# Kernel optimization log

Hardware: AMD Instinct MI355X
Metric: run time of the kernel (lower is better)

## Reference

```python
import jax, jax.numpy as jnp
import numpy as np

B, L, C, H = 4, 2048, 512, 8
D = C // H  # head_dim = 64


def _rope_tables(L, D):
    inv_freq = 1.0 / (10000.0 ** (np.arange(0, D, 2, dtype=np.float32) / D))
    t = np.arange(L, dtype=np.float32)
    freqs = np.outer(t, inv_freq)                      # (L, D/2)
    emb = np.concatenate([freqs, freqs], axis=-1)      # (L, D)
    return jnp.asarray(np.cos(emb)), jnp.asarray(np.sin(emb))


def setup_inputs() -> dict:
    key = jax.random.key(0)
    k1, k2, k3 = jax.random.split(key, 3)
    cos, sin = _rope_tables(L, D)
    return {
        "x": jax.random.normal(k1, (B, L, C), dtype=jnp.float32),
        "qkv_w": jax.random.normal(k2, (3 * C, C), dtype=jnp.float32) * 0.02,
        "qkv_b": jnp.zeros((3 * C,), dtype=jnp.float32),
        "proj_w": jax.random.normal(k3, (C, C), dtype=jnp.float32) * 0.02,
        "proj_b": jnp.zeros((C,), dtype=jnp.float32),
        "cos": cos,
        "sin": sin,
    }


def _rotate_half(x):
    x1, x2 = jnp.split(x, 2, axis=-1)
    return jnp.concatenate([-x2, x1], axis=-1)


def _apply_rope(x, cos, sin):
    # x: (B, H, L, D); cos/sin: (L, D)
    return x * cos[None, None] + _rotate_half(x) * sin[None, None]


def reference(x, qkv_w, qkv_b, proj_w, proj_b, cos, sin):
    b, l, c = x.shape
    scale = 1.0 / jnp.sqrt(jnp.float32(D))
    qkv = x @ qkv_w.T + qkv_b                          # (B, L, 3C)
    qkv = qkv.reshape(b, l, 3, H, D).transpose(2, 0, 3, 1, 4)  # (3, B, H, L, D)
    q, k, v = qkv[0], qkv[1], qkv[2]
    q = _apply_rope(q, cos, sin)
    k = _apply_rope(k, cos, sin)
    attn = jax.nn.softmax(scale * jnp.einsum('bhqd,bhkd->bhqk', q, k), axis=-1)
    out = jnp.einsum('bhqk,bhkd->bhqd', attn, v)       # (B, H, L, D)
    out = out.transpose(0, 2, 1, 3).reshape(b, l, c)   # (B, L, C)
    return out @ proj_w.T + proj_b
```

## Files before the change

### kernel.cpp

```cpp
#include <hip/hip_runtime.h>

#define CDIM 512
#define LDIM 2048
#define BDIM 4
#define HDIM 8
#define DDIM 64

typedef __attribute__((ext_vector_type(8))) short bf16x8;
typedef __attribute__((ext_vector_type(4))) float f32x4;
typedef __attribute__((ext_vector_type(2))) float f32x2;
typedef __attribute__((ext_vector_type(8))) unsigned short ushort8;

static __device__ __forceinline__ unsigned short f2bf(float f) {
  unsigned u = __float_as_uint(f);
  return (unsigned short)((u + 0x7FFFu + ((u >> 16) & 1u)) >> 16);
}

__global__ __launch_bounds__(256) void convert_kernel(
    const float* __restrict__ qw, const float* __restrict__ pw,
    unsigned short* __restrict__ wb, unsigned short* __restrict__ pwb) {
  const size_t i = ((size_t)blockIdx.x * 256 + threadIdx.x) * 8;
  const float* src; unsigned short* dst; size_t off;
  if (i < 786432) { src = qw; dst = wb;  off = i; }
  else            { src = pw; dst = pwb; off = i - 786432; }
  const float4 a = *(const float4*)(src + off);
  const float4 b = *(const float4*)(src + off + 4);
  ushort8 h;
  h[0] = f2bf(a.x); h[1] = f2bf(a.y); h[2] = f2bf(a.z); h[3] = f2bf(a.w);
  h[4] = f2bf(b.x); h[5] = f2bf(b.y); h[6] = f2bf(b.z); h[7] = f2bf(b.w);
  *(ushort8*)(dst + off) = h;
}

__global__ __launch_bounds__(256) void qkv_gemm_kernel(
    const float* __restrict__ x, const unsigned short* __restrict__ wb,
    const float* __restrict__ bias, const float* __restrict__ cosT,
    const float* __restrict__ sinT, unsigned short* __restrict__ qb,
    unsigned short* __restrict__ kb, unsigned short* __restrict__ vt) {
  __shared__ char As[16384];
  __shared__ char Bs[16384];
  const int t  = threadIdx.x;
  const int w  = t >> 6, lane = t & 63;
  const int lo = lane & 15, hi = lane >> 4;
  const int wm = w >> 1, wn = w & 1;
  const int m0 = blockIdx.y * 128, n0 = blockIdx.x * 128;

  f32x4 acc[4][4];
  #pragma unroll
  for (int mt = 0; mt < 4; ++mt)
    #pragma unroll
    for (int nt = 0; nt < 4; ++nt) acc[mt][nt] = (f32x4){0.f, 0.f, 0.f, 0.f};

  const int srow   = t >> 3;
  const int sch    = (t & 7) ^ (srow & 7);
  const char* Bg = (const char*)wb;

  for (int kt = 0; kt < CDIM; kt += 64) {
    #pragma unroll
    for (int s = 0; s < 4; ++s) {
      const int r = s * 32 + srow;
      const float4 f0 = *(const float4*)(x + (size_t)(m0 + r) * CDIM + kt + sch * 8);
      const float4 f1 = *(const float4*)(x + (size_t)(m0 + r) * CDIM + kt + sch * 8 + 4);
      unsigned u0, u1, u2, u3;
      asm("v_cvt_pk_bf16_f32 %0, %1, %2" : "=v"(u0) : "v"(f0.x), "v"(f0.y));
      asm("v_cvt_pk_bf16_f32 %0, %1, %2" : "=v"(u1) : "v"(f0.z), "v"(f0.w));
      asm("v_cvt_pk_bf16_f32 %0, %1, %2" : "=v"(u2) : "v"(f1.x), "v"(f1.y));
      asm("v_cvt_pk_bf16_f32 %0, %1, %2" : "=v"(u3) : "v"(f1.z), "v"(f1.w));
      uint4 uu; uu.x = u0; uu.y = u1; uu.z = u2; uu.w = u3;
      *(uint4*)(As + s * 4096 + t * 16) = uu;
      __builtin_amdgcn_global_load_lds(
          (const __attribute__((address_space(1))) unsigned int*)
              (Bg + (size_t)(n0 + r) * 1024 + kt * 2 + sch * 16),
          (__attribute__((address_space(3))) unsigned int*)(Bs + s * 4096 + w * 1024),
          16, 0, 0);
    }
    __syncthreads();
    #pragma unroll
    for (int ks = 0; ks < 2; ++ks) {
      bf16x8 af[4], bfr[4];
      #pragma unroll
      for (int mt = 0; mt < 4; ++mt)
        af[mt] = *(const bf16x8*)(As + (wm * 64 + mt * 16 + lo) * 128
                                  + (((ks * 4 + hi) ^ (lo & 7)) << 4));
      #pragma unroll
      for (int nt = 0; nt < 4; ++nt)
        bfr[nt] = *(const bf16x8*)(Bs + (wn * 64 + nt * 16 + lo) * 128
                                   + (((ks * 4 + hi) ^ (lo & 7)) << 4));
      #pragma unroll
      for (int mt = 0; mt < 4; ++mt)
        #pragma unroll
        for (int nt = 0; nt < 4; ++nt)
          acc[mt][nt] = __builtin_amdgcn_mfma_f32_16x16x32_bf16(
              af[mt], bfr[nt], acc[mt][nt], 0, 0, 0);
    }
    __syncthreads();
  }

  const int nbase = n0 + wn * 64;
  const int typ   = nbase >> 9;
  const int hh    = (nbase >> 6) & 7;
  const int bb    = m0 >> 11;
  const int lbase = (m0 & 2047) + wm * 64;

  float bq[4];
  #pragma unroll
  for (int nt = 0; nt < 4; ++nt) bq[nt] = bias[nbase + nt * 16 + lo];
  #pragma unroll
  for (int mt = 0; mt < 4; ++mt)
    #pragma unroll
    for (int nt = 0; nt < 4; ++nt)
      #pragma unroll
      for (int reg = 0; reg < 4; ++reg) acc[mt][nt][reg] += bq[nt];

  if (typ == 2) {
    unsigned short* vbase = vt + (size_t)(bb * HDIM + hh) * DDIM * LDIM;
    #pragma unroll
    for (int mt = 0; mt < 4; ++mt)
      #pragma unroll
      for (int nt = 0; nt < 4; ++nt) {
        const int d = nt * 16 + lo;
        #pragma unroll
        for (int reg = 0; reg < 4; ++reg) {
          const int l = lbase + mt * 16 + hi * 4 + reg;
          vbase[(size_t)d * LDIM + l] = f2bf(acc[mt][nt][reg]);
        }
      }
  } else {
    unsigned short* dstb = (typ ? kb : qb) + (size_t)(bb * HDIM + hh) * LDIM * DDIM;
    #pragma unroll
    for (int mt = 0; mt < 4; ++mt)
      #pragma unroll
      for (int nt = 0; nt < 4; ++nt) {
        const int d   = nt * 16 + lo;
        const float sgn = (nt & 2) ? 1.f : -1.f;
        #pragma unroll
        for (int reg = 0; reg < 4; ++reg) {
          const int l = lbase + mt * 16 + hi * 4 + reg;
          const float c = cosT[l * 64 + d], s = sinT[l * 64 + d];
          const float v = acc[mt][nt][reg] * c + sgn * acc[mt][nt ^ 2][reg] * s;
          dstb[(size_t)l * DDIM + d] = f2bf(v);
        }
      }
  }
}

#define CLOG2 0.18033688f

__global__ __launch_bounds__(512, 4) void attn_kernel(
    unsigned short* __restrict__ qb, const unsigned short* __restrict__ kb,
    const unsigned short* __restrict__ vt) {
  __shared__ char Lds[65536];
  const int t    = threadIdx.x;
  const int w    = t >> 6, lane = t & 63;
  const int lo   = lane & 15, hi = lane >> 4;
  const int wq   = w & 3, half = w >> 2;
  const int bh   = blockIdx.y;
  const int q0   = blockIdx.x * 128 + wq * 32;
  const int kb0  = half * 1024;

  const char* Kb = (const char*)kb + (size_t)bh * (LDIM * DDIM * 2);
  const char* Vb = (const char*)vt + (size_t)bh * (LDIM * DDIM * 2);
  unsigned short* Qb = qb + (size_t)bh * (LDIM * DDIM);

  bf16x8 qf[2][2];
  #pragma unroll
  for (int g = 0; g < 2; ++g)
    #pragma unroll
    for (int kd = 0; kd < 2; ++kd)
      qf[g][kd] = *(const bf16x8*)((const char*)(Qb + (size_t)(q0 + g * 16 + lo) * DDIM)
                                   + kd * 64 + hi * 16);

  f32x4 o[2][4];
  float mrun[2] = {0.f, 0.f}, mc[2] = {0.f, 0.f}, lpart[2] = {0.f, 0.f};
  #pragma unroll
  for (int g = 0; g < 2; ++g)
    #pragma unroll
    for (int r = 0; r < 4; ++r) o[g][r] = (f32x4){0.f, 0.f, 0.f, 0.f};

  const int krow = wq * 8 + (lane >> 3);
  const int kch  = ((lane & 7) ^ (krow & 7)) << 4;
  const int vrow = wq * 16 + (lane >> 2);
  const int vch  = ((lane & 3) ^ (vrow & 3)) << 4;

  auto stage = [&](int tile, int buf) {
    __builtin_amdgcn_global_load_lds(
        (const __attribute__((address_space(1))) unsigned int*)
            (Kb + (size_t)(kb0 + tile * 32 + krow) * 128 + kch),
        (__attribute__((address_space(3))) unsigned int*)
            (Lds + (half * 2 + buf) * 4096 + wq * 1024),
        16, 0, 0);
    __builtin_amdgcn_global_load_lds(
        (const __attribute__((address_space(1))) unsigned int*)
            (Vb + (size_t)vrow * (LDIM * 2) + (size_t)(kb0 + tile * 32) * 2 + vch),
        (__attribute__((address_space(3))) unsigned int*)
            (Lds + 16384 + (half * 2 + buf) * 4096 + wq * 1024),
        16, 0, 0);
  };

  stage(0, 0);

  char* Pwb = Lds + 32768 + w * 4096;

  for (int kt = 0; kt < 32; ++kt) {
    const int cur = kt & 1;
    const int nk  = kt < 31 ? kt + 1 : 31;
    stage(nk, cur ^ 1);
    asm volatile("s_waitcnt vmcnt(2)");
    __builtin_amdgcn_s_barrier();
    __builtin_amdgcn_sched_barrier(0);

    const char* Kl = Lds + (half * 2 + cur) * 4096;
    const char* Vl = Lds + 16384 + (half * 2 + cur) * 4096;

    f32x4 sv[2][2];
    __builtin_amdgcn_s_setprio(1);
    #pragma unroll
    for (int nt = 0; nt < 2; ++nt) {
      sv[0][nt] = (f32x4){0.f, 0.f, 0.f, 0.f};
      sv[1][nt] = (f32x4){0.f, 0.f, 0.f, 0.f};
      const int key = nt * 16 + lo;
      #pragma unroll
      for (int kd = 0; kd < 2; ++kd) {
        const bf16x8 kf = *(const bf16x8*)(Kl + key * 128
                            + (((kd * 4 + hi) ^ (lo & 7)) << 4));
        sv[0][nt] = __builtin_amdgcn_mfma_f32_16x16x32_bf16(kf, qf[0][kd], sv[0][nt], 0, 0, 0);
        sv[1][nt] = __builtin_amdgcn_mfma_f32_16x16x32_bf16(kf, qf[1][kd], sv[1][nt], 0, 0, 0);
      }
    }
    __builtin_amdgcn_s_setprio(0);

    #pragma unroll
    for (int g = 0; g < 2; ++g) {
      const float* sflat = (const float*)sv[g];
      const f32x2 cc2 = {CLOG2, CLOG2};
      const f32x2 mm2 = {-mc[g], -mc[g]};
      float pv[8];
      float ps = 0.f;
      #pragma unroll
      for (int i = 0; i < 4; ++i) {
        f32x2 a; a[0] = sflat[2*i]; a[1] = sflat[2*i+1];
        f32x2 xr;
        asm("v_pk_fma_f32 %0, %1, %2, %3" : "=v"(xr) : "v"(a), "v"(cc2), "v"(mm2));
        float p0, p1;
        asm("v_exp_f32 %0, %1" : "=v"(p0) : "v"(xr[0]));
        asm("v_exp_f32 %0, %1" : "=v"(p1) : "v"(xr[1]));
        pv[2*i] = p0; pv[2*i+1] = p1;
        ps += p0; ps += p1;
      }

      if (__builtin_expect((bool)__ballot(ps > 65536.f), 0)) {
        float mx = -1e30f;
        #pragma unroll
        for (int i = 0; i < 8; ++i) mx = fmaxf(mx, sflat[i]);
        mx = fmaxf(mx, __shfl_xor(mx, 16));
        mx = fmaxf(mx, __shfl_xor(mx, 32));
        const float newm = fmaxf(mrun[g], mx);
        const float al   = exp2f((mrun[g] - newm) * CLOG2);
        lpart[g] *= al;
        #pragma unroll
        for (int r = 0; r < 4; ++r) {
          const float aq = __shfl(al, (hi << 2) + r);
          #pragma unroll
          for (int dt = 0; dt < 4; ++dt) o[g][dt][r] *= aq;
        }
        mrun[g] = newm;
        mc[g]   = newm * CLOG2;
        ps = 0.f;
        #pragma unroll
        for (int i = 0; i < 8; ++i) {
          const float p = exp2f(fmaf(sflat[i], CLOG2, -mc[g]));
          pv[i] = p;
          ps += p;
        }
      }
      lpart[g] += ps;

      #pragma unroll
      for (int nt = 0; nt < 2; ++nt) {
        unsigned w0, w1;
        asm("v_cvt_pk_bf16_f32 %0, %1, %2"
            : "=v"(w0) : "v"(pv[nt*4+0]), "v"(pv[nt*4+1]));
        asm("v_cvt_pk_bf16_f32 %0, %1, %2"
            : "=v"(w1) : "v"(pv[nt*4+2]), "v"(pv[nt*4+3]));
        uint2 d2; d2.x = w0; d2.y = w1;
        *(uint2*)(Pwb + g * 2048 + lo * 128
                  + ((nt * 32 + hi * 8) ^ ((lo & 7) << 4))) = d2;
      }
    }

    __builtin_amdgcn_s_setprio(1);
    {
      const bf16x8 pf0 = *(const bf16x8*)(Pwb + lo * 128
                           + ((hi ^ (lo & 7)) << 4));
      const bf16x8 pf1 = *(const bf16x8*)(Pwb + 2048 + lo * 128
                           + ((hi ^ (lo & 7)) << 4));
      #pragma unroll
      for (int dt = 0; dt < 4; ++dt) {
        const int d = dt * 16 + lo;
        const bf16x8 vf = *(const bf16x8*)(Vl + d * 64 + ((hi ^ (lo & 3)) << 4));
        o[0][dt] = __builtin_amdgcn_mfma_f32_16x16x32_bf16(pf0, vf, o[0][dt], 0, 0, 0);
        o[1][dt] = __builtin_amdgcn_mfma_f32_16x16x32_bf16(pf1, vf, o[1][dt], 0, 0, 0);
      }
    }
    __builtin_amdgcn_s_setprio(0);

    __builtin_amdgcn_sched_barrier(0);
    __builtin_amdgcn_s_barrier();
  }

  asm volatile("s_waitcnt vmcnt(0)");
  __syncthreads();

  float rs[2];
  #pragma unroll
  for (int g = 0; g < 2; ++g) {
    rs[g] = lpart[g];
    rs[g] += __shfl_xor(rs[g], 16);
    rs[g] += __shfl_xor(rs[g], 32);
  }

  if (half == 1) {
    #pragma unroll
    for (int g = 0; g < 2; ++g) {
      #pragma unroll
      for (int dt = 0; dt < 4; ++dt)
        #pragma unroll
        for (int r = 0; r < 4; ++r)
          *(float*)(Lds + wq * 8192
                    + ((g * 16 + hi * 4 + r) * 64 + dt * 16 + lo) * 4) = o[g][dt][r];
      if (hi == 0) {
        *(float*)(Lds + 32768 + wq * 256 + g * 64 + lo * 4)       = rs[g];
        *(float*)(Lds + 32768 + wq * 256 + 128 + g * 64 + lo * 4) = mrun[g];
      }
    }
  }
  __syncthreads();
  if (half == 0) {
    #pragma unroll
    for (int g = 0; g < 2; ++g)
      #pragma unroll
      for (int r = 0; r < 4; ++r) {
        const int qrow = hi * 4 + r;
        const float m_a = __shfl(mrun[g], qrow);
        const float l_a = __shfl(rs[g], qrow);
        const float l_b = *(const float*)(Lds + 32768 + wq * 256 + g * 64 + qrow * 4);
        const float m_b = *(const float*)(Lds + 32768 + wq * 256 + 128 + g * 64 + qrow * 4);
        const float m  = fmaxf(m_a, m_b);
        const float aa = exp2f((m_a - m) * CLOG2);
        const float ab = exp2f((m_b - m) * CLOG2);
        const float inv = 1.f / (l_a * aa + l_b * ab);
        const int q = q0 + g * 16 + qrow;
        #pragma unroll
        for (int dt = 0; dt < 4; ++dt) {
          const float ob = *(const float*)(Lds + wq * 8192
                            + ((g * 16 + qrow) * 64 + dt * 16 + lo) * 4);
          Qb[(size_t)q * DDIM + dt * 16 + lo] =
              f2bf((o[g][dt][r] * aa + ob * ab) * inv);
        }
      }
  }
}

__global__ __launch_bounds__(256) void proj_gemm_kernel(
    const unsigned short* __restrict__ ab, const unsigned short* __restrict__ pwb,
    const float* __restrict__ bias, float* __restrict__ out) {
  __shared__ char As[16384];
  __shared__ char Bs[16384];
  const int t  = threadIdx.x;
  const int w  = t >> 6, lane = t & 63;
  const int lo = lane & 15, hi = lane >> 4;
  const int wm = w >> 1, wn = w & 1;
  const int m0 = blockIdx.y * 128, n0 = blockIdx.x * 128;

  f32x4 acc[4][4];
  #pragma unroll
  for (int mt = 0; mt < 4; ++mt)
    #pragma unroll
    for (int nt = 0; nt < 4; ++nt) acc[mt][nt] = (f32x4){0.f, 0.f, 0.f, 0.f};

  const int srow   = t >> 3;
  const int schunk = ((t & 7) ^ (srow & 7)) << 4;
  const char* Ag = (const char*)ab;
  const char* Bg = (const char*)pwb;

  for (int kt = 0; kt < CDIM; kt += 64) {
    const int hh = kt >> 6;
    #pragma unroll
    for (int s = 0; s < 4; ++s) {
      const int r = s * 32 + srow;
      const int m = m0 + r;
      const int bb = m >> 11, l = m & 2047;
      __builtin_amdgcn_global_load_lds(
          (const __attribute__((address_space(1))) unsigned int*)
              (Ag + ((size_t)(bb * HDIM + hh) * LDIM + l) * 128 + schunk),
          (__attribute__((address_space(3))) unsigned int*)(As + s * 4096 + w * 1024),
          16, 0, 0);
      __builtin_amdgcn_global_load_lds(
          (const __attribute__((address_space(1))) unsigned int*)
              (Bg + (size_t)(n0 + r) * 1024 + kt * 2 + schunk),
          (__attribute__((address_space(3))) unsigned int*)(Bs + s * 4096 + w * 1024),
          16, 0, 0);
    }
    __syncthreads();
    #pragma unroll
    for (int ks = 0; ks < 2; ++ks) {
      bf16x8 af[4], bfr[4];
      #pragma unroll
      for (int mt = 0; mt < 4; ++mt)
        af[mt] = *(const bf16x8*)(As + (wm * 64 + mt * 16 + lo) * 128
                                  + (((ks * 4 + hi) ^ (lo & 7)) << 4));
      #pragma unroll
      for (int nt = 0; nt < 4; ++nt)
        bfr[nt] = *(const bf16x8*)(Bs + (wn * 64 + nt * 16 + lo) * 128
                                   + (((ks * 4 + hi) ^ (lo & 7)) << 4));
      #pragma unroll
      for (int mt = 0; mt < 4; ++mt)
        #pragma unroll
        for (int nt = 0; nt < 4; ++nt)
          acc[mt][nt] = __builtin_amdgcn_mfma_f32_16x16x32_bf16(
              af[mt], bfr[nt], acc[mt][nt], 0, 0, 0);
    }
    __syncthreads();
  }

  const int nn = n0 + wn * 64;
  float bp[4];
  #pragma unroll
  for (int nt = 0; nt < 4; ++nt) bp[nt] = bias[nn + nt * 16 + lo];
  #pragma unroll
  for (int mt = 0; mt < 4; ++mt)
    #pragma unroll
    for (int nt = 0; nt < 4; ++nt)
      #pragma unroll
      for (int reg = 0; reg < 4; ++reg) {
        const int m = m0 + wm * 64 + mt * 16 + hi * 4 + reg;
        out[(size_t)m * CDIM + nn + nt * 16 + lo] = acc[mt][nt][reg] + bp[nt];
      }
}

extern "C" void kernel_launch(void* const* d_in, const int* in_sizes, int n_in,
                              void* d_out, int out_size, void* d_ws, size_t ws_size,
                              hipStream_t stream) {
  const float* x      = (const float*)d_in[0];
  const float* qkv_w  = (const float*)d_in[1];
  const float* qkv_b  = (const float*)d_in[2];
  const float* proj_w = (const float*)d_in[3];
  const float* proj_b = (const float*)d_in[4];
  const float* cosT   = (const float*)d_in[5];
  const float* sinT   = (const float*)d_in[6];
  float* out = (float*)d_out;

  unsigned short* qb  = (unsigned short*)d_ws;
  unsigned short* kb  = qb + (size_t)BDIM * HDIM * LDIM * DDIM;
  unsigned short* vt  = kb + (size_t)BDIM * HDIM * LDIM * DDIM;
  unsigned short* wb  = vt + (size_t)BDIM * HDIM * LDIM * DDIM;
  unsigned short* pwb = wb + (size_t)3 * CDIM * CDIM;

  convert_kernel<<<dim3(512), 256, 0, stream>>>(qkv_w, proj_w, wb, pwb);
  qkv_gemm_kernel<<<dim3(12, 64), 256, 0, stream>>>(x, wb, qkv_b, cosT, sinT,
                                                    qb, kb, vt);
  attn_kernel<<<dim3(16, 32), 512, 0, stream>>>(qb, kb, vt);
  proj_gemm_kernel<<<dim3(4, 64), 256, 0, stream>>>(qb, pwb, proj_b, out);
}
```

Measured before the change: 107.7 us.

## Pre-convert x to bf16, async-load A tiles, reswizzle V LDS, halve proj tile

x is now converted to bf16 once in the convert kernel, so the QKV GEMM can stage A tiles through direct global-to-LDS loads instead of loading fp32, converting in registers and storing to LDS. That cuts per-tile conversion work and redundant fp32 reads, since each x tile was read by 12 column blocks, at the cost of an extra bf16 write and read of x. The V tile LDS swizzle is changed to use (row>>1)&3 to reduce bank conflicts. The projection GEMM uses 64-row M tiles with twice as many blocks to improve occupancy and wave count.

Result: faster. 97.28 us (-9.7%).

```diff
diff --git a/kernel.cpp b/kernel.cpp
--- a/kernel.cpp
+++ b/kernel.cpp
@@ -17,12 +17,14 @@
 }
 
 __global__ __launch_bounds__(256) void convert_kernel(
-    const float* __restrict__ qw, const float* __restrict__ pw,
+    const float* __restrict__ x, const float* __restrict__ qw,
+    const float* __restrict__ pw, unsigned short* __restrict__ xb,
     unsigned short* __restrict__ wb, unsigned short* __restrict__ pwb) {
   const size_t i = ((size_t)blockIdx.x * 256 + threadIdx.x) * 8;
   const float* src; unsigned short* dst; size_t off;
-  if (i < 786432) { src = qw; dst = wb;  off = i; }
-  else            { src = pw; dst = pwb; off = i - 786432; }
+  if (i < 4194304) { src = x;  dst = xb;  off = i; }
+  else if (i < 4980736) { src = qw; dst = wb;  off = i - 4194304; }
+  else { src = pw; dst = pwb; off = i - 4980736; }
   const float4 a = *(const float4*)(src + off);
   const float4 b = *(const float4*)(src + off + 4);
   ushort8 h;
@@ -32,7 +34,7 @@
 }
 
 __global__ __launch_bounds__(256) void qkv_gemm_kernel(
-    const float* __restrict__ x, const unsigned short* __restrict__ wb,
+    const unsigned short* __restrict__ xb, const unsigned short* __restrict__ wb,
     const float* __restrict__ bias, const float* __restrict__ cosT,
     const float* __restrict__ sinT, unsigned short* __restrict__ qb,
     unsigned short* __restrict__ kb, unsigned short* __restrict__ vt) {
@@ -51,25 +53,22 @@
     for (int nt = 0; nt < 4; ++nt) acc[mt][nt] = (f32x4){0.f, 0.f, 0.f, 0.f};
 
   const int srow   = t >> 3;
-  const int sch    = (t & 7) ^ (srow & 7);
+  const int schunk = ((t & 7) ^ (srow & 7)) << 4;
+  const char* Ag = (const char*)xb;
   const char* Bg = (const char*)wb;
 
   for (int kt = 0; kt < CDIM; kt += 64) {
     #pragma unroll
     for (int s = 0; s < 4; ++s) {
       const int r = s * 32 + srow;
-      const float4 f0 = *(const float4*)(x + (size_t)(m0 + r) * CDIM + kt + sch * 8);
-      const float4 f1 = *(const float4*)(x + (size_t)(m0 + r) * CDIM + kt + sch * 8 + 4);
-      unsigned u0, u1, u2, u3;
-      asm("v_cvt_pk_bf16_f32 %0, %1, %2" : "=v"(u0) : "v"(f0.x), "v"(f0.y));
-      asm("v_cvt_pk_bf16_f32 %0, %1, %2" : "=v"(u1) : "v"(f0.z), "v"(f0.w));
-      asm("v_cvt_pk_bf16_f32 %0, %1, %2" : "=v"(u2) : "v"(f1.x), "v"(f1.y));
-      asm("v_cvt_pk_bf16_f32 %0, %1, %2" : "=v"(u3) : "v"(f1.z), "v"(f1.w));
-      uint4 uu; uu.x = u0; uu.y = u1; uu.z = u2; uu.w = u3;
-      *(uint4*)(As + s * 4096 + t * 16) = uu;
       __builtin_amdgcn_global_load_lds(
           (const __attribute__((address_space(1))) unsigned int*)
-              (Bg + (size_t)(n0 + r) * 1024 + kt * 2 + sch * 16),
+              (Ag + (size_t)(m0 + r) * 1024 + kt * 2 + schunk),
+          (__attribute__((address_space(3))) unsigned int*)(As + s * 4096 + w * 1024),
+          16, 0, 0);
+      __builtin_amdgcn_global_load_lds(
+          (const __attribute__((address_space(1))) unsigned int*)
+              (Bg + (size_t)(n0 + r) * 1024 + kt * 2 + schunk),
           (__attribute__((address_space(3))) unsigned int*)(Bs + s * 4096 + w * 1024),
           16, 0, 0);
     }
@@ -179,7 +178,7 @@
   const int krow = wq * 8 + (lane >> 3);
   const int kch  = ((lane & 7) ^ (krow & 7)) << 4;
   const int vrow = wq * 16 + (lane >> 2);
-  const int vch  = ((lane & 3) ^ (vrow & 3)) << 4;
+  const int vch  = ((lane & 3) ^ ((vrow >> 1) & 3)) << 4;
 
   auto stage = [&](int tile, int buf) {
     __builtin_amdgcn_global_load_lds(
@@ -296,7 +295,8 @@
       #pragma unroll
       for (int dt = 0; dt < 4; ++dt) {
         const int d = dt * 16 + lo;
-        const bf16x8 vf = *(const bf16x8*)(Vl + d * 64 + ((hi ^ (lo & 3)) << 4));
+        const bf16x8 vf = *(const bf16x8*)(Vl + d * 64
+                            + ((hi ^ ((d >> 1) & 3)) << 4));
         o[0][dt] = __builtin_amdgcn_mfma_f32_16x16x32_bf16(pf0, vf, o[0][dt], 0, 0, 0);
         o[1][dt] = __builtin_amdgcn_mfma_f32_16x16x32_bf16(pf1, vf, o[1][dt], 0, 0, 0);
       }
@@ -363,17 +363,17 @@
 __global__ __launch_bounds__(256) void proj_gemm_kernel(
     const unsigned short* __restrict__ ab, const unsigned short* __restrict__ pwb,
     const float* __restrict__ bias, float* __restrict__ out) {
-  __shared__ char As[16384];
+  __shared__ char As[8192];
   __shared__ char Bs[16384];
   const int t  = threadIdx.x;
   const int w  = t >> 6, lane = t & 63;
   const int lo = lane & 15, hi = lane >> 4;
   const int wm = w >> 1, wn = w & 1;
-  const int m0 = blockIdx.y * 128, n0 = blockIdx.x * 128;
-
-  f32x4 acc[4][4];
-  #pragma unroll
-  for (int mt = 0; mt < 4; ++mt)
+  const int m0 = blockIdx.y * 64, n0 = blockIdx.x * 128;
+
+  f32x4 acc[2][4];
+  #pragma unroll
+  for (int mt = 0; mt < 2; ++mt)
     #pragma unroll
     for (int nt = 0; nt < 4; ++nt) acc[mt][nt] = (f32x4){0.f, 0.f, 0.f, 0.f};
 
@@ -385,7 +385,7 @@
   for (int kt = 0; kt < CDIM; kt += 64) {
     const int hh = kt >> 6;
     #pragma unroll
-    for (int s = 0; s < 4; ++s) {
+    for (int s = 0; s < 2; ++s) {
       const int r = s * 32 + srow;
       const int m = m0 + r;
       const int bb = m >> 11, l = m & 2047;
@@ -394,6 +394,10 @@
               (Ag + ((size_t)(bb * HDIM + hh) * LDIM + l) * 128 + schunk),
           (__attribute__((address_space(3))) unsigned int*)(As + s * 4096 + w * 1024),
           16, 0, 0);
+    }
+    #pragma unroll
+    for (int s = 0; s < 4; ++s) {
+      const int r = s * 32 + srow;
       __builtin_amdgcn_global_load_lds(
           (const __attribute__((address_space(1))) unsigned int*)
               (Bg + (size_t)(n0 + r) * 1024 + kt * 2 + schunk),
@@ -403,17 +407,17 @@
     __syncthreads();
     #pragma unroll
     for (int ks = 0; ks < 2; ++ks) {
-      bf16x8 af[4], bfr[4];
-      #pragma unroll
-      for (int mt = 0; mt < 4; ++mt)
-        af[mt] = *(const bf16x8*)(As + (wm * 64 + mt * 16 + lo) * 128
+      bf16x8 af[2], bfr[4];
+      #pragma unroll
+      for (int mt = 0; mt < 2; ++mt)
+        af[mt] = *(const bf16x8*)(As + (wm * 32 + mt * 16 + lo) * 128
                                   + (((ks * 4 + hi) ^ (lo & 7)) << 4));
       #pragma unroll
       for (int nt = 0; nt < 4; ++nt)
         bfr[nt] = *(const bf16x8*)(Bs + (wn * 64 + nt * 16 + lo) * 128
                                    + (((ks * 4 + hi) ^ (lo & 7)) << 4));
       #pragma unroll
-      for (int mt = 0; mt < 4; ++mt)
+      for (int mt = 0; mt < 2; ++mt)
         #pragma unroll
         for (int nt = 0; nt < 4; ++nt)
           acc[mt][nt] = __builtin_amdgcn_mfma_f32_16x16x32_bf16(
@@ -427,12 +431,12 @@
   #pragma unroll
   for (int nt = 0; nt < 4; ++nt) bp[nt] = bias[nn + nt * 16 + lo];
   #pragma unroll
-  for (int mt = 0; mt < 4; ++mt)
+  for (int mt = 0; mt < 2; ++mt)
     #pragma unroll
     for (int nt = 0; nt < 4; ++nt)
       #pragma unroll
       for (int reg = 0; reg < 4; ++reg) {
-        const int m = m0 + wm * 64 + mt * 16 + hi * 4 + reg;
+        const int m = m0 + wm * 32 + mt * 16 + hi * 4 + reg;
         out[(size_t)m * CDIM + nn + nt * 16 + lo] = acc[mt][nt][reg] + bp[nt];
       }
 }
@@ -452,12 +456,13 @@
   unsigned short* qb  = (unsigned short*)d_ws;
   unsigned short* kb  = qb + (size_t)BDIM * HDIM * LDIM * DDIM;
   unsigned short* vt  = kb + (size_t)BDIM * HDIM * LDIM * DDIM;
-  unsigned short* wb  = vt + (size_t)BDIM * HDIM * LDIM * DDIM;
+  unsigned short* xb  = vt + (size_t)BDIM * HDIM * LDIM * DDIM;
+  unsigned short* wb  = xb + (size_t)BDIM * LDIM * CDIM;
   unsigned short* pwb = wb + (size_t)3 * CDIM * CDIM;
 
-  convert_kernel<<<dim3(512), 256, 0, stream>>>(qkv_w, proj_w, wb, pwb);
-  qkv_gemm_kernel<<<dim3(12, 64), 256, 0, stream>>>(x, wb, qkv_b, cosT, sinT,
+  convert_kernel<<<dim3(2560), 256, 0, stream>>>(x, qkv_w, proj_w, xb, wb, pwb);
+  qkv_gemm_kernel<<<dim3(12, 64), 256, 0, stream>>>(xb, wb, qkv_b, cosT, sinT,
                                                     qb, kb, vt);
   attn_kernel<<<dim3(16, 32), 512, 0, stream>>>(qb, kb, vt);
-  proj_gemm_kernel<<<dim3(4, 64), 256, 0, stream>>>(qb, pwb, proj_b, out);
-}
+  proj_gemm_kernel<<<dim3(4, 128), 256, 0, stream>>>(qb, pwb, proj_b, out);
+}
```
